# Performance work log

Measured on AMD Instinct MI355X. Metric: run time of the kernel, lower is better.

The kernel has to match this reference:

```python
import jax, jax.numpy as jnp
import numpy as np

D_MODEL = 1024
D_FF = 4096


def _layernorm(x, g, b, eps=1e-5):
    mu = jnp.mean(x, axis=-1, keepdims=True)
    var = jnp.var(x, axis=-1, keepdims=True)
    return (x - mu) * jax.lax.rsqrt(var + eps) * g + b


def setup_inputs() -> dict:
    key = jax.random.key(0)
    ks = jax.random.split(key, 16)
    d, f = D_MODEL, D_FF
    s = 1.0 / np.sqrt(d)
    inp = {
        'x': jax.random.normal(ks[0], (4, 2048, d), dtype=jnp.float32),
        'wq': jax.random.uniform(ks[1], (d, d), jnp.float32, -s, s),
        'bq': jax.random.uniform(ks[2], (d,), jnp.float32, -s, s),
        'wk': jax.random.uniform(ks[3], (d, d), jnp.float32, -s, s),
        'bk': jax.random.uniform(ks[4], (d,), jnp.float32, -s, s),
        'wv': jax.random.uniform(ks[5], (d, d), jnp.float32, -s, s),
        'bv': jax.random.uniform(ks[6], (d,), jnp.float32, -s, s),
        'wo': jax.random.uniform(ks[7], (d, d), jnp.float32, -s, s),
        'bo': jax.random.uniform(ks[8], (d,), jnp.float32, -s, s),
        'w1': jax.random.uniform(ks[9], (d, f), jnp.float32, -s, s),
        'b1': jax.random.uniform(ks[10], (f,), jnp.float32, -s, s),
        'w2': jax.random.uniform(ks[11], (f, d), jnp.float32, -1.0 / np.sqrt(f), 1.0 / np.sqrt(f)),
        'b2': jax.random.uniform(ks[12], (d,), jnp.float32, -1.0 / np.sqrt(f), 1.0 / np.sqrt(f)),
        'g1': jnp.ones((d,), jnp.float32),
        'be1': jnp.zeros((d,), jnp.float32),
        'g2': jnp.ones((d,), jnp.float32),
        'be2': jnp.zeros((d,), jnp.float32),
    }
    return inp


def reference(x, wq, bq, wk, bk, wv, bv, wo, bo, w1, b1, w2, b2, g1, be1, g2, be2):
    d_k = x.shape[-1]
    q = jnp.einsum('bsd,de->bse', x, wq) + bq
    k = jnp.einsum('bsd,de->bse', x, wk) + bk
    v = jnp.einsum('bsd,de->bse', x, wv) + bv
    # full-width attention (no head split in the original module)
    scores = jnp.einsum('bqd,bkd->bqk', q, k) / jnp.sqrt(jnp.float32(d_k))
    attn = jax.nn.softmax(scores, axis=-1)
    ctx = jnp.einsum('bqk,bkd->bqd', attn, v)
    attn_out = jnp.einsum('bsd,de->bse', ctx, wo) + bo
    x1 = _layernorm(x + attn_out, g1, be1)
    ff = jnp.einsum('bsf,fd->bsd', jax.nn.relu(jnp.einsum('bsd,df->bsf', x1, w1) + b1), w2) + b2
    return _layernorm(x1 + ff, g2, be2)
```

## Files before the change

kernel.cpp:

```cpp
#include <hip/hip_runtime.h>
#include <stdint.h>


using f32x4 = __attribute__((ext_vector_type(4))) float;
using s16x8 = __attribute__((ext_vector_type(8))) short;

__device__ __forceinline__ ushort f2b(float f) {
    union { float f; uint32_t u; } v; v.f = f;
    uint32_t u = v.u;
    return (ushort)((u + 0x7fffu + ((u >> 16) & 1u)) >> 16);
}
__device__ __forceinline__ float b2f(ushort b) {
    union { uint32_t u; float f; } v; v.u = ((uint32_t)b) << 16;
    return v.f;
}
__device__ __forceinline__ float to_f(float f) { return f; }
__device__ __forceinline__ float to_f(ushort b) { return b2f(b); }

__device__ __forceinline__ void async_ld16(const ushort* g, ushort* l) {
    __builtin_amdgcn_global_load_lds(
        (const __attribute__((address_space(1))) void*)g,
        (__attribute__((address_space(3))) void*)l,
        16, 0, 0);
}


__global__ __launch_bounds__(256) void cast_f2b4(const float* __restrict__ src,
                                                 ushort* __restrict__ dst,
                                                 long long n4) {
    long long i = (long long)blockIdx.x * 256 + threadIdx.x;
    if (i >= n4) return;
    float4 f = ((const float4*)src)[i];
    ushort4 o;
    o.x = f2b(f.x); o.y = f2b(f.y); o.z = f2b(f.z); o.w = f2b(f.w);
    ((ushort4*)dst)[i] = o;
}


template <typename T>
__global__ __launch_bounds__(256) void transpose_to_bf16(const T* __restrict__ src,
                                                         ushort* __restrict__ dst,
                                                         int R, int C,
                                                         long long ss, long long ds) {
    __shared__ float tile[32][33];
    src += (long long)blockIdx.z * ss;
    dst += (long long)blockIdx.z * ds;
    const int c0 = blockIdx.x * 32;
    const int r0 = blockIdx.y * 32;
    const int tx = threadIdx.x, ty = threadIdx.y;
#pragma unroll
    for (int i = 0; i < 4; i++) {
        int r = r0 + ty + i * 8;
        tile[ty + i * 8][tx] = to_f(src[(long long)r * C + c0 + tx]);
    }
    __syncthreads();
#pragma unroll
    for (int i = 0; i < 4; i++) {
        int r = c0 + ty + i * 8;
        dst[(long long)r * R + r0 + tx] = f2b(tile[tx][ty + i * 8]);
    }
}


#define BM 128
#define BN 128
#define BKK 32

template <int OUT_BF16, int RELU, int HAS_BIAS>
__global__ __launch_bounds__(256) void gemm_bt(const ushort* __restrict__ A,
                                               const ushort* __restrict__ BT,
                                               void* __restrict__ Cp,
                                               const float* __restrict__ bias,
                                               int M, int N, int K, float scale,
                                               long long sA, long long sB, long long sC) {
    __shared__ ushort As[BM * BKK];
    __shared__ ushort Bs[BN * BKK];

    const int tid = threadIdx.x;
    const int bz = blockIdx.z;
    const ushort* Ab = A + (long long)bz * sA;
    const ushort* Bb = BT + (long long)bz * sB;

    const int tm = blockIdx.y;
    const int tn = blockIdx.x;

    const int lane = tid & 63;
    const int wave = tid >> 6;
    const int wm = (wave >> 1) * 64;
    const int wn = (wave & 1) * 64;
    const int quad = lane >> 4;
    const int l16 = lane & 15;

    const int srow = wave * 32 + (lane >> 2);
    const int scol = (lane & 3) * 8;
    const ushort* AgL = Ab + (long long)(tm * BM + srow) * K + scol;
    const ushort* BgL = Bb + (long long)(tn * BN + srow) * K + scol;
    ushort* AsL = As + wave * 1024;
    ushort* BsL = Bs + wave * 1024;
    const long long rstep = (long long)16 * K;

    f32x4 acc[4][4];
#pragma unroll
    for (int i = 0; i < 4; i++)
#pragma unroll
        for (int j = 0; j < 4; j++) acc[i][j] = (f32x4){0.f, 0.f, 0.f, 0.f};

    for (int k0 = 0; k0 < K; k0 += BKK) {
        async_ld16(AgL + k0, AsL);
        async_ld16(AgL + rstep + k0, AsL + 512);
        async_ld16(BgL + k0, BsL);
        async_ld16(BgL + rstep + k0, BsL + 512);
        __syncthreads();

        s16x8 af[4], bf[4];
#pragma unroll
        for (int i = 0; i < 4; i++)
            af[i] = *(const s16x8*)&As[(wm + i * 16 + l16) * BKK + quad * 8];
#pragma unroll
        for (int j = 0; j < 4; j++)
            bf[j] = *(const s16x8*)&Bs[(wn + j * 16 + l16) * BKK + quad * 8];
#pragma unroll
        for (int i = 0; i < 4; i++)
#pragma unroll
            for (int j = 0; j < 4; j++)
                acc[i][j] = __builtin_amdgcn_mfma_f32_16x16x32_bf16(af[i], bf[j], acc[i][j], 0, 0, 0);
        __syncthreads();
    }

    const long long cb = (long long)bz * sC;
    float* Cf = (float*)Cp;
    ushort* Cb = (ushort*)Cp;
#pragma unroll
    for (int j = 0; j < 4; j++) {
        const int col = tn * BN + wn + j * 16 + l16;
        float bv = HAS_BIAS ? bias[col] : 0.0f;
#pragma unroll
        for (int i = 0; i < 4; i++) {
            const int row0 = tm * BM + wm + i * 16 + quad * 4;
#pragma unroll
            for (int r = 0; r < 4; r++) {
                float v = acc[i][j][r] * scale + bv;
                if (RELU) v = v > 0.f ? v : 0.f;
                long long idx = cb + (long long)(row0 + r) * N + col;
                if (OUT_BF16) Cb[idx] = f2b(v);
                else Cf[idx] = v;
            }
        }
    }
}


__global__ __launch_bounds__(256) void softmax_rows(const float* __restrict__ S,
                                                    ushort* __restrict__ P) {
    const int C = 2048;
    const long long row = blockIdx.x;
    const float* s = S + row * C;
    ushort* p = P + row * C;
    const int tid = threadIdx.x;
    float v[8];
    float mx = -1e30f;
#pragma unroll
    for (int i = 0; i < 8; i++) {
        v[i] = s[tid + i * 256];
        mx = fmaxf(mx, v[i]);
    }
    __shared__ float red[256];
    red[tid] = mx;
    __syncthreads();
    for (int off = 128; off > 0; off >>= 1) {
        if (tid < off) red[tid] = fmaxf(red[tid], red[tid + off]);
        __syncthreads();
    }
    mx = red[0];
    __syncthreads();
    float sum = 0.f;
#pragma unroll
    for (int i = 0; i < 8; i++) {
        v[i] = __expf(v[i] - mx);
        sum += v[i];
    }
    red[tid] = sum;
    __syncthreads();
    for (int off = 128; off > 0; off >>= 1) {
        if (tid < off) red[tid] += red[tid + off];
        __syncthreads();
    }
    float inv = 1.f / red[0];
#pragma unroll
    for (int i = 0; i < 8; i++) p[tid + i * 256] = f2b(v[i] * inv);
}


__global__ __launch_bounds__(256) void residual_ln(const float* __restrict__ X,
                                                   const float* __restrict__ Y,
                                                   const float* __restrict__ g,
                                                   const float* __restrict__ be,
                                                   float* __restrict__ outf,
                                                   ushort* __restrict__ outb) {
    const int D = 1024;
    const long long row = blockIdx.x;
    const float* x = X + row * D;
    const float* y = Y + row * D;
    const int tid = threadIdx.x;
    float v[4];
    float s = 0.f, s2 = 0.f;
#pragma unroll
    for (int i = 0; i < 4; i++) {
        int c = tid + i * 256;
        float t = x[c] + y[c];
        v[i] = t;
        s += t;
        s2 += t * t;
    }
    __shared__ float r1[256], r2[256];
    r1[tid] = s;
    r2[tid] = s2;
    __syncthreads();
    for (int off = 128; off > 0; off >>= 1) {
        if (tid < off) {
            r1[tid] += r1[tid + off];
            r2[tid] += r2[tid + off];
        }
        __syncthreads();
    }
    float mu = r1[0] * (1.f / 1024.f);
    float var = r2[0] * (1.f / 1024.f) - mu * mu;
    float inv = rsqrtf(var + 1e-5f);
    float* of = outf + row * D;
    ushort* ob = outb ? outb + row * D : nullptr;
#pragma unroll
    for (int i = 0; i < 4; i++) {
        int c = tid + i * 256;
        float o = (v[i] - mu) * inv * g[c] + be[c];
        of[c] = o;
        if (ob) ob[c] = f2b(o);
    }
}


extern "C" void kernel_launch(void* const* d_in, const int* in_sizes, int n_in,
                              void* d_out, int out_size, void* d_ws, size_t ws_size,
                              hipStream_t stream) {
    const float* x  = (const float*)d_in[0];
    const float* wq = (const float*)d_in[1];
    const float* bq = (const float*)d_in[2];
    const float* wk = (const float*)d_in[3];
    const float* bk = (const float*)d_in[4];
    const float* wv = (const float*)d_in[5];
    const float* bv = (const float*)d_in[6];
    const float* wo = (const float*)d_in[7];
    const float* bo = (const float*)d_in[8];
    const float* w1 = (const float*)d_in[9];
    const float* b1 = (const float*)d_in[10];
    const float* w2 = (const float*)d_in[11];
    const float* b2 = (const float*)d_in[12];
    const float* g1 = (const float*)d_in[13];
    const float* be1 = (const float*)d_in[14];
    const float* g2 = (const float*)d_in[15];
    const float* be2 = (const float*)d_in[16];
    float* out = (float*)d_out;
    char* ws = (char*)d_ws;

    const int Bz = 4, S = 2048, D = 1024, F = 4096;
    const int T = Bz * S;
    const size_t MBy = 1024ull * 1024ull;

    ushort* xb  = (ushort*)(ws + 0);
    ushort* wqT = (ushort*)(ws + 16 * MBy);
    ushort* wkT = (ushort*)(ws + 18 * MBy);
    ushort* wvT = (ushort*)(ws + 20 * MBy);
    ushort* woT = (ushort*)(ws + 22 * MBy);
    ushort* w1T = (ushort*)(ws + 24 * MBy);
    ushort* w2T = (ushort*)(ws + 32 * MBy);
    ushort* qb  = (ushort*)(ws + 40 * MBy);
    ushort* kb  = (ushort*)(ws + 56 * MBy);
    ushort* vb  = (ushort*)(ws + 72 * MBy);
    ushort* vT  = (ushort*)(ws + 88 * MBy);
    float*  sc  = (float*)(ws + 104 * MBy);
    ushort* attn = (ushort*)(ws + 168 * MBy);
    ushort* ctx = (ushort*)(ws + 40 * MBy);
    float*  ao  = (float*)(ws + 104 * MBy);
    float*  x1  = (float*)(ws + 56 * MBy);
    ushort* x1b = (ushort*)(ws + 88 * MBy);
    ushort* h   = (ushort*)(ws + 104 * MBy);
    float*  ff  = (float*)(ws + 168 * MBy);

    dim3 b32(32, 8);

    cast_f2b4<<<(T * D) / 1024, 256, 0, stream>>>(x, xb, (long long)(T * D) / 4);

    transpose_to_bf16<float><<<dim3(32, 32, 1), b32, 0, stream>>>(wq, wqT, D, D, 0, 0);
    transpose_to_bf16<float><<<dim3(32, 32, 1), b32, 0, stream>>>(wk, wkT, D, D, 0, 0);
    transpose_to_bf16<float><<<dim3(32, 32, 1), b32, 0, stream>>>(wv, wvT, D, D, 0, 0);
    transpose_to_bf16<float><<<dim3(32, 32, 1), b32, 0, stream>>>(wo, woT, D, D, 0, 0);
    transpose_to_bf16<float><<<dim3(128, 32, 1), b32, 0, stream>>>(w1, w1T, D, F, 0, 0);
    transpose_to_bf16<float><<<dim3(32, 128, 1), b32, 0, stream>>>(w2, w2T, F, D, 0, 0);

    gemm_bt<1, 0, 1><<<dim3(D / 128, T / 128, 1), 256, 0, stream>>>(xb, wqT, qb, bq, T, D, D, 1.f, 0, 0, 0);
    gemm_bt<1, 0, 1><<<dim3(D / 128, T / 128, 1), 256, 0, stream>>>(xb, wkT, kb, bk, T, D, D, 1.f, 0, 0, 0);
    gemm_bt<1, 0, 1><<<dim3(D / 128, T / 128, 1), 256, 0, stream>>>(xb, wvT, vb, bv, T, D, D, 1.f, 0, 0, 0);

    transpose_to_bf16<ushort><<<dim3(D / 32, S / 32, Bz), b32, 0, stream>>>(
        vb, vT, S, D, (long long)S * D, (long long)S * D);

    gemm_bt<0, 0, 0><<<dim3(S / 128, S / 128, Bz), 256, 0, stream>>>(
        qb, kb, sc, nullptr, S, S, D, 0.03125f,
        (long long)S * D, (long long)S * D, (long long)S * S);

    softmax_rows<<<T, 256, 0, stream>>>(sc, attn);

    gemm_bt<1, 0, 0><<<dim3(D / 128, S / 128, Bz), 256, 0, stream>>>(
        attn, vT, ctx, nullptr, S, D, S, 1.f,
        (long long)S * S, (long long)D * S, (long long)S * D);

    gemm_bt<0, 0, 1><<<dim3(D / 128, T / 128, 1), 256, 0, stream>>>(ctx, woT, ao, bo, T, D, D, 1.f, 0, 0, 0);

    residual_ln<<<T, 256, 0, stream>>>(x, ao, g1, be1, x1, x1b);

    gemm_bt<1, 1, 1><<<dim3(F / 128, T / 128, 1), 256, 0, stream>>>(x1b, w1T, h, b1, T, F, D, 1.f, 0, 0, 0);

    gemm_bt<0, 0, 1><<<dim3(D / 128, T / 128, 1), 256, 0, stream>>>(h, w2T, ff, b2, T, D, F, 1.f, 0, 0, 0);

    residual_ln<<<T, 256, 0, stream>>>(x1, ff, g2, be2, out, nullptr);
}
```

Before: 670.3 us.

## Fuse QKV projections, add XCD-aware tile mapping and split-K atomics

Q, K and V projections become one GEMM over a concatenated transposed weight with strided outputs, and later kernels read Q/K/V in place through leading-dimension parameters. The block-to-tile mapping is swizzled so consecutive blocks on the same XCD share an M-band, aiming for better L2 reuse. The Wo and W2 GEMMs use split-K with float atomic adds into zeroed buffers to raise block count. This adds zeroing kernels and atomic traffic, and the float summation order is no longer deterministic.

```diff
diff --git a/kernel.cpp b/kernel.cpp
--- a/kernel.cpp
+++ b/kernel.cpp
@@ -37,10 +37,17 @@
 }
 
 
+__global__ __launch_bounds__(256) void zero_f4(float* __restrict__ dst, long long n4) {
+    long long i = (long long)blockIdx.x * 256 + threadIdx.x;
+    if (i >= n4) return;
+    ((float4*)dst)[i] = (float4){0.f, 0.f, 0.f, 0.f};
+}
+
+
 template <typename T>
 __global__ __launch_bounds__(256) void transpose_to_bf16(const T* __restrict__ src,
                                                          ushort* __restrict__ dst,
-                                                         int R, int C,
+                                                         int R, int C, int srcLd,
                                                          long long ss, long long ds) {
     __shared__ float tile[32][33];
     src += (long long)blockIdx.z * ss;
@@ -51,7 +58,7 @@
 #pragma unroll
     for (int i = 0; i < 4; i++) {
         int r = r0 + ty + i * 8;
-        tile[ty + i * 8][tx] = to_f(src[(long long)r * C + c0 + tx]);
+        tile[ty + i * 8][tx] = to_f(src[(long long)r * srcLd + c0 + tx]);
     }
     __syncthreads();
 #pragma unroll
@@ -66,23 +73,32 @@
 #define BN 128
 #define BKK 32
 
-template <int OUT_BF16, int RELU, int HAS_BIAS>
+template <int OUT_BF16, int RELU, int HAS_BIAS, int ATOMIC>
 __global__ __launch_bounds__(256) void gemm_bt(const ushort* __restrict__ A,
                                                const ushort* __restrict__ BT,
                                                void* __restrict__ Cp,
                                                const float* __restrict__ bias,
-                                               int M, int N, int K, float scale,
+                                               int N, int K, int kChunks, float scale,
+                                               int lda, int ldb, int ldc,
                                                long long sA, long long sB, long long sC) {
     __shared__ ushort As[BM * BKK];
     __shared__ ushort Bs[BN * BKK];
 
     const int tid = threadIdx.x;
-    const int bz = blockIdx.z;
+    const int kIdx = blockIdx.z % kChunks;
+    const int bz = blockIdx.z / kChunks;
+    const int kLen = K / kChunks;
+    const int kOff = kIdx * kLen;
     const ushort* Ab = A + (long long)bz * sA;
     const ushort* Bb = BT + (long long)bz * sB;
 
-    const int tm = blockIdx.y;
-    const int tn = blockIdx.x;
+    const int W = gridDim.x, H = gridDim.y;
+    const int b = blockIdx.y * W + blockIdx.x;
+    const int Hp = H >> 3;
+    const int xcd = b & 7;
+    const int s = b >> 3;
+    const int tn = s / Hp;
+    const int tm = xcd * Hp + (s % Hp);
 
     const int lane = tid & 63;
     const int wave = tid >> 6;
@@ -93,11 +109,12 @@
 
     const int srow = wave * 32 + (lane >> 2);
     const int scol = (lane & 3) * 8;
-    const ushort* AgL = Ab + (long long)(tm * BM + srow) * K + scol;
-    const ushort* BgL = Bb + (long long)(tn * BN + srow) * K + scol;
+    const ushort* AgL = Ab + (long long)(tm * BM + srow) * lda + scol + kOff;
+    const ushort* BgL = Bb + (long long)(tn * BN + srow) * ldb + scol + kOff;
     ushort* AsL = As + wave * 1024;
     ushort* BsL = Bs + wave * 1024;
-    const long long rstep = (long long)16 * K;
+    const long long rstepA = (long long)16 * lda;
+    const long long rstepB = (long long)16 * ldb;
 
     f32x4 acc[4][4];
 #pragma unroll
@@ -105,11 +122,11 @@
 #pragma unroll
         for (int j = 0; j < 4; j++) acc[i][j] = (f32x4){0.f, 0.f, 0.f, 0.f};
 
-    for (int k0 = 0; k0 < K; k0 += BKK) {
+    for (int k0 = 0; k0 < kLen; k0 += BKK) {
         async_ld16(AgL + k0, AsL);
-        async_ld16(AgL + rstep + k0, AsL + 512);
+        async_ld16(AgL + rstepA + k0, AsL + 512);
         async_ld16(BgL + k0, BsL);
-        async_ld16(BgL + rstep + k0, BsL + 512);
+        async_ld16(BgL + rstepB + k0, BsL + 512);
         __syncthreads();
 
         s16x8 af[4], bf[4];
@@ -133,7 +150,7 @@
 #pragma unroll
     for (int j = 0; j < 4; j++) {
         const int col = tn * BN + wn + j * 16 + l16;
-        float bv = HAS_BIAS ? bias[col] : 0.0f;
+        float bv = (HAS_BIAS && (!ATOMIC || kIdx == 0)) ? bias[col] : 0.0f;
 #pragma unroll
         for (int i = 0; i < 4; i++) {
             const int row0 = tm * BM + wm + i * 16 + quad * 4;
@@ -141,8 +158,9 @@
             for (int r = 0; r < 4; r++) {
                 float v = acc[i][j][r] * scale + bv;
                 if (RELU) v = v > 0.f ? v : 0.f;
-                long long idx = cb + (long long)(row0 + r) * N + col;
-                if (OUT_BF16) Cb[idx] = f2b(v);
+                long long idx = cb + (long long)(row0 + r) * ldc + col;
+                if (ATOMIC) unsafeAtomicAdd(&Cf[idx], v);
+                else if (OUT_BF16) Cb[idx] = f2b(v);
                 else Cf[idx] = v;
             }
         }
@@ -265,18 +283,15 @@
     const int T = Bz * S;
     const size_t MBy = 1024ull * 1024ull;
 
-    ushort* xb  = (ushort*)(ws + 0);
-    ushort* wqT = (ushort*)(ws + 16 * MBy);
-    ushort* wkT = (ushort*)(ws + 18 * MBy);
-    ushort* wvT = (ushort*)(ws + 20 * MBy);
-    ushort* woT = (ushort*)(ws + 22 * MBy);
-    ushort* w1T = (ushort*)(ws + 24 * MBy);
-    ushort* w2T = (ushort*)(ws + 32 * MBy);
-    ushort* qb  = (ushort*)(ws + 40 * MBy);
-    ushort* kb  = (ushort*)(ws + 56 * MBy);
-    ushort* vb  = (ushort*)(ws + 72 * MBy);
-    ushort* vT  = (ushort*)(ws + 88 * MBy);
-    float*  sc  = (float*)(ws + 104 * MBy);
+    ushort* xb   = (ushort*)(ws + 0);
+    ushort* qkvT = (ushort*)(ws + 16 * MBy);
+    ushort* woT  = (ushort*)(ws + 22 * MBy);
+    ushort* w1T  = (ushort*)(ws + 24 * MBy);
+    ushort* w2T  = (ushort*)(ws + 32 * MBy);
+    ushort* qkv  = (ushort*)(ws + 40 * MBy);
+    ushort* vT   = (ushort*)(ws + 88 * MBy);
+    float*  bqkv = (float*)(ws + 104 * MBy);
+    float*  sc   = (float*)(ws + 104 * MBy);
     ushort* attn = (ushort*)(ws + 168 * MBy);
     ushort* ctx = (ushort*)(ws + 40 * MBy);
     float*  ao  = (float*)(ws + 104 * MBy);
@@ -289,37 +304,47 @@
 
     cast_f2b4<<<(T * D) / 1024, 256, 0, stream>>>(x, xb, (long long)(T * D) / 4);
 
-    transpose_to_bf16<float><<<dim3(32, 32, 1), b32, 0, stream>>>(wq, wqT, D, D, 0, 0);
-    transpose_to_bf16<float><<<dim3(32, 32, 1), b32, 0, stream>>>(wk, wkT, D, D, 0, 0);
-    transpose_to_bf16<float><<<dim3(32, 32, 1), b32, 0, stream>>>(wv, wvT, D, D, 0, 0);
-    transpose_to_bf16<float><<<dim3(32, 32, 1), b32, 0, stream>>>(wo, woT, D, D, 0, 0);
-    transpose_to_bf16<float><<<dim3(128, 32, 1), b32, 0, stream>>>(w1, w1T, D, F, 0, 0);
-    transpose_to_bf16<float><<<dim3(32, 128, 1), b32, 0, stream>>>(w2, w2T, F, D, 0, 0);
-
-    gemm_bt<1, 0, 1><<<dim3(D / 128, T / 128, 1), 256, 0, stream>>>(xb, wqT, qb, bq, T, D, D, 1.f, 0, 0, 0);
-    gemm_bt<1, 0, 1><<<dim3(D / 128, T / 128, 1), 256, 0, stream>>>(xb, wkT, kb, bk, T, D, D, 1.f, 0, 0, 0);
-    gemm_bt<1, 0, 1><<<dim3(D / 128, T / 128, 1), 256, 0, stream>>>(xb, wvT, vb, bv, T, D, D, 1.f, 0, 0, 0);
+    transpose_to_bf16<float><<<dim3(32, 32, 1), b32, 0, stream>>>(wq, qkvT, D, D, D, 0, 0);
+    transpose_to_bf16<float><<<dim3(32, 32, 1), b32, 0, stream>>>(wk, qkvT + 1024 * 1024, D, D, D, 0, 0);
+    transpose_to_bf16<float><<<dim3(32, 32, 1), b32, 0, stream>>>(wv, qkvT + 2048 * 1024, D, D, D, 0, 0);
+    transpose_to_bf16<float><<<dim3(32, 32, 1), b32, 0, stream>>>(wo, woT, D, D, D, 0, 0);
+    transpose_to_bf16<float><<<dim3(128, 32, 1), b32, 0, stream>>>(w1, w1T, D, F, F, 0, 0);
+    transpose_to_bf16<float><<<dim3(32, 128, 1), b32, 0, stream>>>(w2, w2T, F, D, D, 0, 0);
+
+    hipMemcpyAsync(bqkv, bq, D * sizeof(float), hipMemcpyDeviceToDevice, stream);
+    hipMemcpyAsync(bqkv + D, bk, D * sizeof(float), hipMemcpyDeviceToDevice, stream);
+    hipMemcpyAsync(bqkv + 2 * D, bv, D * sizeof(float), hipMemcpyDeviceToDevice, stream);
+
+    gemm_bt<1, 0, 1, 0><<<dim3(3 * D / 128, T / 128, 1), 256, 0, stream>>>(
+        xb, qkvT, qkv, bqkv, 3 * D, D, 1, 1.f, D, D, 3 * D, 0, 0, 0);
 
     transpose_to_bf16<ushort><<<dim3(D / 32, S / 32, Bz), b32, 0, stream>>>(
-        vb, vT, S, D, (long long)S * D, (long long)S * D);
-
-    gemm_bt<0, 0, 0><<<dim3(S / 128, S / 128, Bz), 256, 0, stream>>>(
-        qb, kb, sc, nullptr, S, S, D, 0.03125f,
-        (long long)S * D, (long long)S * D, (long long)S * S);
+        qkv + 2048, vT, S, D, 3 * D, (long long)S * 3 * D, (long long)S * D);
+
+    gemm_bt<0, 0, 0, 0><<<dim3(S / 128, S / 128, Bz), 256, 0, stream>>>(
+        qkv, qkv + 1024, sc, nullptr, S, D, 1, 0.03125f, 3 * D, 3 * D, S,
+        (long long)S * 3 * D, (long long)S * 3 * D, (long long)S * S);
 
     softmax_rows<<<T, 256, 0, stream>>>(sc, attn);
 
-    gemm_bt<1, 0, 0><<<dim3(D / 128, S / 128, Bz), 256, 0, stream>>>(
-        attn, vT, ctx, nullptr, S, D, S, 1.f,
+    zero_f4<<<(T * D) / 1024, 256, 0, stream>>>(ao, (long long)(T * D) / 4);
+
+    gemm_bt<1, 0, 0, 0><<<dim3(D / 128, S / 128, Bz), 256, 0, stream>>>(
+        attn, vT, ctx, nullptr, D, S, 1, 1.f, S, S, D,
         (long long)S * S, (long long)D * S, (long long)S * D);
 
-    gemm_bt<0, 0, 1><<<dim3(D / 128, T / 128, 1), 256, 0, stream>>>(ctx, woT, ao, bo, T, D, D, 1.f, 0, 0, 0);
+    gemm_bt<0, 0, 1, 1><<<dim3(D / 128, T / 128, 2), 256, 0, stream>>>(
+        ctx, woT, ao, bo, D, D, 2, 1.f, D, D, D, 0, 0, 0);
 
     residual_ln<<<T, 256, 0, stream>>>(x, ao, g1, be1, x1, x1b);
 
-    gemm_bt<1, 1, 1><<<dim3(F / 128, T / 128, 1), 256, 0, stream>>>(x1b, w1T, h, b1, T, F, D, 1.f, 0, 0, 0);
-
-    gemm_bt<0, 0, 1><<<dim3(D / 128, T / 128, 1), 256, 0, stream>>>(h, w2T, ff, b2, T, D, F, 1.f, 0, 0, 0);
+    zero_f4<<<(T * D) / 1024, 256, 0, stream>>>(ff, (long long)(T * D) / 4);
+
+    gemm_bt<1, 1, 1, 0><<<dim3(F / 128, T / 128, 1), 256, 0, stream>>>(
+        x1b, w1T, h, b1, F, D, 1, 1.f, D, D, F, 0, 0, 0);
+
+    gemm_bt<0, 0, 1, 1><<<dim3(D / 128, T / 128, 4), 256, 0, stream>>>(
+        h, w2T, ff, b2, D, F, 4, 1.f, F, F, D, 0, 0, 0);
 
     residual_ln<<<T, 256, 0, stream>>>(x1, ff, g2, be2, out, nullptr);
 }
```

Result: slower. 748.6 us (+11.7%).
